# Optimization experiments

Measured on AMD Instinct MI355X. Metric: run time of the kernel, lower is better.

Reference implementation:

```python
import jax, jax.numpy as jnp
import numpy as np

B, C, W, H = 16, 512, 32, 32


def spatial_shift1(y):
    # y: [B, W, H, C]; quartile-wise shifts with edge rows/cols left unchanged
    c = y.shape[-1]
    cq = c // 4
    p0 = jnp.concatenate([y[:, :1, :, 0*cq:1*cq], y[:, :-1, :, 0*cq:1*cq]], axis=1)  # w <- w-1
    p1 = jnp.concatenate([y[:, 1:, :, 1*cq:2*cq], y[:, -1:, :, 1*cq:2*cq]], axis=1)  # w <- w+1
    p2 = jnp.concatenate([y[:, :, :1, 2*cq:3*cq], y[:, :, :-1, 2*cq:3*cq]], axis=2)  # h <- h-1
    p3 = jnp.concatenate([y[:, :, 1:, 3*cq:], y[:, :, -1:, 3*cq:]], axis=2)          # h <- h+1
    return jnp.concatenate([p0, p1, p2, p3], axis=-1)


def spatial_shift2(y):
    # same as shift1 with w/h roles swapped
    c = y.shape[-1]
    cq = c // 4
    p0 = jnp.concatenate([y[:, :, :1, 0*cq:1*cq], y[:, :, :-1, 0*cq:1*cq]], axis=2)  # h <- h-1
    p1 = jnp.concatenate([y[:, :, 1:, 1*cq:2*cq], y[:, :, -1:, 1*cq:2*cq]], axis=2)  # h <- h+1
    p2 = jnp.concatenate([y[:, :1, :, 2*cq:3*cq], y[:, :-1, :, 2*cq:3*cq]], axis=1)  # w <- w-1
    p3 = jnp.concatenate([y[:, 1:, :, 3*cq:], y[:, -1:, :, 3*cq:]], axis=1)          # w <- w+1
    return jnp.concatenate([p0, p1, p2, p3], axis=-1)


def setup_inputs() -> dict:
    key = jax.random.key(0)
    ks = jax.random.split(key, 9)
    s = 0.02
    return {
        "x": jax.random.normal(ks[0], (B, C, W, H), dtype=jnp.float32),
        "w1": jax.random.normal(ks[1], (3 * C, C), dtype=jnp.float32) * s,
        "b1": jax.random.normal(ks[2], (3 * C,), dtype=jnp.float32) * s,
        "wa": jax.random.normal(ks[3], (C, C), dtype=jnp.float32) * s,
        "ba": jax.random.normal(ks[4], (C,), dtype=jnp.float32) * s,
        "wb": jax.random.normal(ks[5], (3 * C, C), dtype=jnp.float32) * s,
        "bb": jax.random.normal(ks[6], (3 * C,), dtype=jnp.float32) * s,
        "w2": jax.random.normal(ks[7], (C, C), dtype=jnp.float32) * s,
        "b2": jax.random.normal(ks[8], (C,), dtype=jnp.float32) * s,
    }


def reference(x, w1, b1, wa, ba, wb, bb, w2, b2):
    c = x.shape[1]
    xp = jnp.transpose(x, (0, 2, 3, 1))                     # [B, W, H, C]
    y = jnp.einsum("bwhc,oc->bwho", xp, w1) + b1            # [B, W, H, 3C]
    x1 = spatial_shift1(y[..., :c])
    x2 = spatial_shift2(y[..., c:2 * c])
    x3 = y[..., 2 * c:]
    # SplitAttention: descriptor a = sum over branches and spatial positions
    a = jnp.sum(x1 + x2 + x3, axis=(1, 2))                  # [B, C]
    hat = jax.nn.gelu(a @ wa.T + ba, approximate=False) @ wb.T + bb  # [B, 3C]
    bar = jax.nn.softmax(hat.reshape(-1, 3, c), axis=1)     # softmax over k=3
    g = bar[:, :, None, None, :]                            # [B, 3, 1, 1, C]
    out = g[:, 0] * x1 + g[:, 1] * x2 + g[:, 2] * x3        # [B, W, H, C]
    z = jnp.einsum("bwhc,oc->bwho", out, w2) + b2           # [B, W, H, C]
    return jnp.transpose(z, (0, 3, 1, 2))                   # [B, C, W, H]
```

## Files before the change

### kernel.cpp

```cpp
#include <hip/hip_runtime.h>
#include <stdint.h>

typedef __bf16 bf16x8 __attribute__((ext_vector_type(8)));
typedef float f32x4 __attribute__((ext_vector_type(4)));

#define B_ 16
#define C_ 512
#define S_ 1024
#define N1 1536

__device__ inline unsigned short f2b(float f) {
    unsigned int u = __builtin_bit_cast(unsigned int, f);
    unsigned int lsb = (u >> 16) & 1u;
    u += 0x7fffu + lsb;
    return (unsigned short)(u >> 16);
}
__device__ inline float b2f(unsigned int s) {
    unsigned int u = (s & 0xffffu) << 16;
    return __builtin_bit_cast(float, u);
}

__device__ inline void gl_lds16(const unsigned short* g, unsigned short* l) {
    __builtin_amdgcn_global_load_lds(
        (const __attribute__((address_space(1))) void*)(g),
        (__attribute__((address_space(3))) void*)(l),
        16, 0, 0);
}

__global__ void transpose_convert_x(const float* __restrict__ x, unsigned short* __restrict__ xT) {
    __shared__ float tile[32][33];
    int b = blockIdx.z;
    int c0 = blockIdx.y * 32;
    int s0 = blockIdx.x * 32;
    int tx = threadIdx.x, ty = threadIdx.y;
    const float* xp = x + ((size_t)b * C_ + c0) * S_ + s0;
#pragma unroll
    for (int i = 0; i < 4; i++)
        tile[ty + i * 8][tx] = xp[(size_t)(ty + i * 8) * S_ + tx];
    __syncthreads();
    unsigned short* op = xT + ((size_t)b * S_ + s0) * C_ + c0;
#pragma unroll
    for (int i = 0; i < 4; i++)
        op[(size_t)(ty + i * 8) * C_ + tx] = f2b(tile[tx][ty + i * 8]);
}

__global__ __launch_bounds__(256) void misc_prep(
    const float* __restrict__ w1, const float* __restrict__ w2,
    unsigned short* __restrict__ w1b, unsigned short* __restrict__ w2b,
    float* __restrict__ sums)
{
    int i = blockIdx.x * 256 + threadIdx.x;
    if (i < 196608) {
        float4 v = ((const float4*)w1)[i];
        ((ushort4*)w1b)[i] = make_ushort4(f2b(v.x), f2b(v.y), f2b(v.z), f2b(v.w));
    } else if (i < 262144) {
        int j = i - 196608;
        float4 v = ((const float4*)w2)[j];
        ((ushort4*)w2b)[j] = make_ushort4(f2b(v.x), f2b(v.y), f2b(v.z), f2b(v.w));
    } else if (i < 292864) {
        int j = i - 262144;
        ((float4*)sums)[j] = make_float4(0.f, 0.f, 0.f, 0.f);
    }
}

template <bool TRANS_OUT, bool DO_SUMS>
__global__ __launch_bounds__(256) void gemm_bf16(
    const unsigned short* __restrict__ A,
    const unsigned short* __restrict__ Wt,
    const float* __restrict__ bias,
    void* __restrict__ Cout, int N,
    float* __restrict__ Tsum, float* __restrict__ H0, float* __restrict__ H31,
    float* __restrict__ C0, float* __restrict__ C31)
{
    const int K = 512;
    __shared__ __align__(16) unsigned short As[128 * 32];
    __shared__ __align__(16) unsigned short Bs[128 * 32];
    int m0 = blockIdx.x * 128;
    int n0 = blockIdx.y * 128;
    int tid = threadIdx.x;
    int lane = tid & 63, wid = tid >> 6;
    int wm = (wid >> 1) * 64, wn = (wid & 1) * 64;
    int quad = lane >> 4, l16 = lane & 15;
    int ch0 = wid * 128 + lane;
    const unsigned short* Ab = A + (size_t)m0 * K;
    const unsigned short* Bb = Wt + (size_t)n0 * K;

    f32x4 acc[4][4] = {};

    for (int kt = 0; kt < K; kt += 32) {
        __syncthreads();
#pragma unroll
        for (int i = 0; i < 2; i++) {
            int ch = ch0 + i * 64;
            int m = ch >> 2, kc = ch & 3;
            size_t go = (size_t)m * K + kt + kc * 8;
            gl_lds16(Ab + go, &As[ch * 8]);
            gl_lds16(Bb + go, &Bs[ch * 8]);
        }
        __syncthreads();
        bf16x8 af[4], bfr[4];
#pragma unroll
        for (int t = 0; t < 4; t++) {
            af[t]  = *(const bf16x8*)&As[(wm + t * 16 + l16) * 32 + quad * 8];
            bfr[t] = *(const bf16x8*)&Bs[(wn + t * 16 + l16) * 32 + quad * 8];
        }
#pragma unroll
        for (int mt = 0; mt < 4; mt++)
#pragma unroll
            for (int nt = 0; nt < 4; nt++)
                acc[mt][nt] = __builtin_amdgcn_mfma_f32_16x16x32_bf16(af[mt], bfr[nt], acc[mt][nt], 0, 0, 0);
    }

#pragma unroll
    for (int mt = 0; mt < 4; mt++) {
#pragma unroll
        for (int nt = 0; nt < 4; nt++) {
            int n = n0 + wn + nt * 16 + l16;
            float bv = bias[n];
            int mbase = m0 + wm + mt * 16 + quad * 4;
            if (!TRANS_OUT) {
                unsigned short* Y = (unsigned short*)Cout;
#pragma unroll
                for (int r = 0; r < 4; r++)
                    Y[(size_t)(mbase + r) * N + n] = f2b(acc[mt][nt][r] + bv);
            } else {
                float* Z = (float*)Cout;
                int b = mbase >> 10;
                int s = mbase & 1023;
                float4 v = make_float4(acc[mt][nt][0] + bv, acc[mt][nt][1] + bv,
                                       acc[mt][nt][2] + bv, acc[mt][nt][3] + bv);
                *(float4*)(&Z[((size_t)(b * 512 + n)) * 1024 + s]) = v;
            }
        }
    }

    if (DO_SUMS) {
        int b = m0 >> 10;
        int wlo = (m0 & 1023) >> 5;
#pragma unroll
        for (int nt = 0; nt < 4; nt++) {
            int n = n0 + wn + nt * 16 + l16;
            float bv = bias[n];
            float tT = 0.f;
#pragma unroll
            for (int mt = 0; mt < 4; mt++)
#pragma unroll
                for (int r = 0; r < 4; r++) tT += acc[mt][nt][r] + bv;
            tT += __shfl_xor(tT, 16);
            tT += __shfl_xor(tT, 32);
            if (quad == 0) {
                atomicAdd(&Tsum[b * 1536 + n], tT);
                float th0 = acc[0][nt][0] + acc[2][nt][0] + 2.f * bv;
                atomicAdd(&H0[b * 1536 + n], th0);
            }
            if (quad == 3) {
                float th31 = acc[1][nt][3] + acc[3][nt][3] + 2.f * bv;
                atomicAdd(&H31[b * 1536 + n], th31);
            }
            if (wlo == 0 && wm == 0) {
                float tc = 0.f;
#pragma unroll
                for (int mt = 0; mt < 2; mt++)
#pragma unroll
                    for (int r = 0; r < 4; r++) tc += acc[mt][nt][r] + bv;
                tc += __shfl_xor(tc, 16);
                tc += __shfl_xor(tc, 32);
                if (quad == 0) atomicAdd(&C0[b * 1536 + n], tc);
            }
            if (wlo == 28 && wm == 64) {
                float tc = 0.f;
#pragma unroll
                for (int mt = 2; mt < 4; mt++)
#pragma unroll
                    for (int r = 0; r < 4; r++) tc += acc[mt][nt][r] + bv;
                tc += __shfl_xor(tc, 16);
                tc += __shfl_xor(tc, 32);
                if (quad == 0) atomicAdd(&C31[b * 1536 + n], tc);
            }
        }
    }
}

__global__ __launch_bounds__(256) void mlp_layer1(
    const float* __restrict__ sums, const float* __restrict__ wa,
    const float* __restrict__ ba, float* __restrict__ h)
{
    __shared__ float sa[512];
    int b = blockIdx.x >> 7;
    int t = threadIdx.x;
    const float* Tp   = sums;
    const float* H0p  = sums + 24576;
    const float* H31p = sums + 49152;
    const float* C0p  = sums + 73728;
    const float* C31p = sums + 98304;
#pragma unroll
    for (int j = 0; j < 2; j++) {
        int c = t + j * 256;
        int q = c >> 7;
        int n1 = b * 1536 + c;
        float t123 = Tp[n1] + Tp[n1 + 512] + Tp[n1 + 1024];
        float sC1 = C0p[n1] - C31p[n1];
        float sH1 = H0p[n1] - H31p[n1];
        float sC2 = C0p[n1 + 512] - C31p[n1 + 512];
        float sH2 = H0p[n1 + 512] - H31p[n1 + 512];
        float e = (q < 2) ? (sC1 + sH2) : (sH1 + sC2);
        sa[c] = t123 + ((q & 1) ? -e : e);
    }
    __syncthreads();
    int lane = t & 63, wid = t >> 6;
    int o = (blockIdx.x & 127) * 4 + wid;
    const float4* wr = (const float4*)(wa + (size_t)o * 512);
    float4 w0 = wr[lane * 2], w1v = wr[lane * 2 + 1];
    float4 a0 = ((const float4*)sa)[lane * 2], a1 = ((const float4*)sa)[lane * 2 + 1];
    float dot = w0.x * a0.x + w0.y * a0.y + w0.z * a0.z + w0.w * a0.w
              + w1v.x * a1.x + w1v.y * a1.y + w1v.z * a1.z + w1v.w * a1.w;
#pragma unroll
    for (int off = 32; off; off >>= 1) dot += __shfl_down(dot, off);
    if (lane == 0) {
        float v = dot + ba[o];
        h[b * 512 + o] = 0.5f * v * (1.0f + erff(v * 0.7071067811865475f));
    }
}

__global__ __launch_bounds__(256) void mlp_layer2(
    const float* __restrict__ h, const float* __restrict__ wb,
    const float* __restrict__ bb, float* __restrict__ hat)
{
    int gw = (blockIdx.x * 256 + threadIdx.x) >> 6;
    int lane = threadIdx.x & 63;
    int b = gw / 1536;
    int o = gw - b * 1536;
    const float4* wr = (const float4*)(wb + (size_t)o * 512);
    const float4* hr = (const float4*)(h + (size_t)b * 512);
    float4 w0 = wr[lane * 2], w1 = wr[lane * 2 + 1];
    float4 h0 = hr[lane * 2], h1 = hr[lane * 2 + 1];
    float dot = w0.x * h0.x + w0.y * h0.y + w0.z * h0.z + w0.w * h0.w
              + w1.x * h1.x + w1.y * h1.y + w1.z * h1.z + w1.w * h1.w;
#pragma unroll
    for (int off = 32; off; off >>= 1) dot += __shfl_down(dot, off);
    if (lane == 0)
        hat[(size_t)b * 1536 + o] = dot + bb[o];
}

__global__ __launch_bounds__(256) void combine_softmax(
    const unsigned short* __restrict__ y, const float* __restrict__ hat,
    unsigned short* __restrict__ outT)
{
    int b = blockIdx.y;
    int t = threadIdx.x;
    int w = blockIdx.x * 4 + (t >> 6);
    int c8 = (t & 63) * 8;
    int q = c8 >> 7;
    int dw1 = (q == 0) ? -1 : (q == 1) ? 1 : 0;
    int dh1 = (q == 2) ? -1 : (q == 3) ? 1 : 0;
    int dh2 = (q == 0) ? -1 : (q == 1) ? 1 : 0;
    int dw2 = (q == 2) ? -1 : (q == 3) ? 1 : 0;
    float g0[8], g1[8], g2[8];
#pragma unroll
    for (int j = 0; j < 8; j++) {
        int c = c8 + j;
        float h0 = hat[b * 1536 + c];
        float h1 = hat[b * 1536 + 512 + c];
        float h2 = hat[b * 1536 + 1024 + c];
        float mx = fmaxf(h0, fmaxf(h1, h2));
        float e0 = __expf(h0 - mx), e1 = __expf(h1 - mx), e2 = __expf(h2 - mx);
        float inv = 1.0f / (e0 + e1 + e2);
        g0[j] = e0 * inv; g1[j] = e1 * inv; g2[j] = e2 * inv;
    }
    int w1i = min(max(w + dw1, 0), 31);
    int w2i = min(max(w + dw2, 0), 31);
    size_t base = (size_t)b * S_;
    for (int h = 0; h < 32; h++) {
        int h1i = min(max(h + dh1, 0), 31);
        int h2i = min(max(h + dh2, 0), 31);
        uint4 u1 = *(const uint4*)&y[(base + w1i * 32 + h1i) * N1 + c8];
        uint4 u2 = *(const uint4*)&y[(base + w2i * 32 + h2i) * N1 + 512 + c8];
        uint4 u3 = *(const uint4*)&y[(base + w * 32 + h) * N1 + 1024 + c8];
        unsigned int p[4];
        const unsigned int* a1 = &u1.x;
        const unsigned int* a2 = &u2.x;
        const unsigned int* a3 = &u3.x;
#pragma unroll
        for (int k = 0; k < 4; k++) {
            int j = k * 2;
            float lo = g0[j] * b2f(a1[k]) + g1[j] * b2f(a2[k]) + g2[j] * b2f(a3[k]);
            float hi = g0[j + 1] * b2f(a1[k] >> 16) + g1[j + 1] * b2f(a2[k] >> 16) + g2[j + 1] * b2f(a3[k] >> 16);
            p[k] = (unsigned int)f2b(lo) | ((unsigned int)f2b(hi) << 16);
        }
        *(uint4*)&outT[(base + w * 32 + h) * 512 + c8] = make_uint4(p[0], p[1], p[2], p[3]);
    }
}

extern "C" void kernel_launch(void* const* d_in, const int* in_sizes, int n_in,
                              void* d_out, int out_size, void* d_ws, size_t ws_size,
                              hipStream_t stream) {
    const float* x  = (const float*)d_in[0];
    const float* w1 = (const float*)d_in[1];
    const float* b1 = (const float*)d_in[2];
    const float* wa = (const float*)d_in[3];
    const float* ba = (const float*)d_in[4];
    const float* wb = (const float*)d_in[5];
    const float* bb = (const float*)d_in[6];
    const float* w2 = (const float*)d_in[7];
    const float* b2 = (const float*)d_in[8];
    float* out = (float*)d_out;

    char* ws = (char*)d_ws;
    unsigned short* xT   = (unsigned short*)(ws);
    unsigned short* outT = (unsigned short*)(ws);
    unsigned short* w1b  = (unsigned short*)(ws + 16777216);
    unsigned short* w2b  = (unsigned short*)(ws + 18350080);
    unsigned short* y    = (unsigned short*)(ws + 18874368);
    float* sums          = (float*)(ws + 69206016);
    float* h_buf         = (float*)(ws + 69697536);
    float* hat_buf       = (float*)(ws + 69730304);

    float* Tsum = sums;
    float* H0   = sums + 24576;
    float* H31  = sums + 49152;
    float* C0   = sums + 73728;
    float* C31  = sums + 98304;

    transpose_convert_x<<<dim3(32, 16, 16), dim3(32, 8), 0, stream>>>(x, xT);
    misc_prep<<<dim3(1144), dim3(256), 0, stream>>>(w1, w2, w1b, w2b, sums);
    gemm_bf16<false, true><<<dim3(128, 12), dim3(256), 0, stream>>>(
        xT, w1b, b1, (void*)y, 1536, Tsum, H0, H31, C0, C31);
    mlp_layer1<<<dim3(2048), dim3(256), 0, stream>>>(sums, wa, ba, h_buf);
    mlp_layer2<<<dim3(6144), dim3(256), 0, stream>>>(h_buf, wb, bb, hat_buf);
    combine_softmax<<<dim3(8, 16), dim3(256), 0, stream>>>(y, hat_buf, outT);
    gemm_bf16<true, false><<<dim3(128, 4), dim3(256), 0, stream>>>(
        outT, w2b, b2, (void*)out, 512, nullptr, nullptr, nullptr, nullptr, nullptr);
}
```

Measured before the change: 194.5 us.

## Widen GEMM K-tile with XOR-swizzled LDS, fuse prep kernels, parallelize combine

The GEMM now stages a 64-wide K slice per iteration and applies an XOR swizzle to the LDS layout. This halves the number of barrier pairs and is meant to avoid LDS bank conflicts on fragment reads. The weight-conversion and zeroing work is folded into the transpose kernel as an extra grid slice, which removes one kernel launch. combine_softmax now launches 4x more blocks, each covering 8 h-rows per wave instead of 32, to raise occupancy, at the cost of recomputing the softmax gates more often.

```diff
diff --git a/kernel.cpp b/kernel.cpp
--- a/kernel.cpp
+++ b/kernel.cpp
@@ -27,7 +27,29 @@
         16, 0, 0);
 }
 
-__global__ void transpose_convert_x(const float* __restrict__ x, unsigned short* __restrict__ xT) {
+__global__ void transpose_convert_x(const float* __restrict__ x, unsigned short* __restrict__ xT,
+                                    const float* __restrict__ w1, const float* __restrict__ w2,
+                                    unsigned short* __restrict__ w1b, unsigned short* __restrict__ w2b,
+                                    float* __restrict__ sums) {
+    if (blockIdx.z == 16) {
+        int t = (blockIdx.y * 32 + blockIdx.x) * 256 + threadIdx.y * 32 + threadIdx.x;
+#pragma unroll
+        for (int it = 0; it < 3; it++) {
+            int i = t + it * 131072;
+            if (i < 196608) {
+                float4 v = ((const float4*)w1)[i];
+                ((ushort4*)w1b)[i] = make_ushort4(f2b(v.x), f2b(v.y), f2b(v.z), f2b(v.w));
+            } else if (i < 262144) {
+                int j = i - 196608;
+                float4 v = ((const float4*)w2)[j];
+                ((ushort4*)w2b)[j] = make_ushort4(f2b(v.x), f2b(v.y), f2b(v.z), f2b(v.w));
+            } else if (i < 292864) {
+                int j = i - 262144;
+                ((float4*)sums)[j] = make_float4(0.f, 0.f, 0.f, 0.f);
+            }
+        }
+        return;
+    }
     __shared__ float tile[32][33];
     int b = blockIdx.z;
     int c0 = blockIdx.y * 32;
@@ -42,25 +64,6 @@
 #pragma unroll
     for (int i = 0; i < 4; i++)
         op[(size_t)(ty + i * 8) * C_ + tx] = f2b(tile[tx][ty + i * 8]);
-}
-
-__global__ __launch_bounds__(256) void misc_prep(
-    const float* __restrict__ w1, const float* __restrict__ w2,
-    unsigned short* __restrict__ w1b, unsigned short* __restrict__ w2b,
-    float* __restrict__ sums)
-{
-    int i = blockIdx.x * 256 + threadIdx.x;
-    if (i < 196608) {
-        float4 v = ((const float4*)w1)[i];
-        ((ushort4*)w1b)[i] = make_ushort4(f2b(v.x), f2b(v.y), f2b(v.z), f2b(v.w));
-    } else if (i < 262144) {
-        int j = i - 196608;
-        float4 v = ((const float4*)w2)[j];
-        ((ushort4*)w2b)[j] = make_ushort4(f2b(v.x), f2b(v.y), f2b(v.z), f2b(v.w));
-    } else if (i < 292864) {
-        int j = i - 262144;
-        ((float4*)sums)[j] = make_float4(0.f, 0.f, 0.f, 0.f);
-    }
 }
 
 template <bool TRANS_OUT, bool DO_SUMS>
@@ -73,42 +76,48 @@
     float* __restrict__ C0, float* __restrict__ C31)
 {
     const int K = 512;
-    __shared__ __align__(16) unsigned short As[128 * 32];
-    __shared__ __align__(16) unsigned short Bs[128 * 32];
+    __shared__ __align__(16) unsigned short As[128 * 64];
+    __shared__ __align__(16) unsigned short Bs[128 * 64];
     int m0 = blockIdx.x * 128;
     int n0 = blockIdx.y * 128;
     int tid = threadIdx.x;
     int lane = tid & 63, wid = tid >> 6;
     int wm = (wid >> 1) * 64, wn = (wid & 1) * 64;
     int quad = lane >> 4, l16 = lane & 15;
-    int ch0 = wid * 128 + lane;
     const unsigned short* Ab = A + (size_t)m0 * K;
     const unsigned short* Bb = Wt + (size_t)n0 * K;
 
     f32x4 acc[4][4] = {};
 
-    for (int kt = 0; kt < K; kt += 32) {
+    for (int kt = 0; kt < K; kt += 64) {
         __syncthreads();
 #pragma unroll
-        for (int i = 0; i < 2; i++) {
-            int ch = ch0 + i * 64;
-            int m = ch >> 2, kc = ch & 3;
+        for (int i = 0; i < 4; i++) {
+            int ch = i * 256 + tid;
+            int m = ch >> 3;
+            int kc = (ch & 7) ^ (m & 7);
             size_t go = (size_t)m * K + kt + kc * 8;
             gl_lds16(Ab + go, &As[ch * 8]);
             gl_lds16(Bb + go, &Bs[ch * 8]);
         }
         __syncthreads();
-        bf16x8 af[4], bfr[4];
-#pragma unroll
-        for (int t = 0; t < 4; t++) {
-            af[t]  = *(const bf16x8*)&As[(wm + t * 16 + l16) * 32 + quad * 8];
-            bfr[t] = *(const bf16x8*)&Bs[(wn + t * 16 + l16) * 32 + quad * 8];
-        }
-#pragma unroll
-        for (int mt = 0; mt < 4; mt++)
-#pragma unroll
-            for (int nt = 0; nt < 4; nt++)
-                acc[mt][nt] = __builtin_amdgcn_mfma_f32_16x16x32_bf16(af[mt], bfr[nt], acc[mt][nt], 0, 0, 0);
+#pragma unroll
+        for (int kh = 0; kh < 2; kh++) {
+            bf16x8 af[4], bfr[4];
+#pragma unroll
+            for (int t = 0; t < 4; t++) {
+                int ra = wm + t * 16 + l16;
+                int rb = wn + t * 16 + l16;
+                int kq = kh * 4 + quad;
+                af[t]  = *(const bf16x8*)&As[ra * 64 + ((kq ^ (ra & 7)) * 8)];
+                bfr[t] = *(const bf16x8*)&Bs[rb * 64 + ((kq ^ (rb & 7)) * 8)];
+            }
+#pragma unroll
+            for (int mt = 0; mt < 4; mt++)
+#pragma unroll
+                for (int nt = 0; nt < 4; nt++)
+                    acc[mt][nt] = __builtin_amdgcn_mfma_f32_16x16x32_bf16(af[mt], bfr[nt], acc[mt][nt], 0, 0, 0);
+        }
     }
 
 #pragma unroll
@@ -247,8 +256,9 @@
     unsigned short* __restrict__ outT)
 {
     int b = blockIdx.y;
+    int w = blockIdx.x;
     int t = threadIdx.x;
-    int w = blockIdx.x * 4 + (t >> 6);
+    int h0 = (t >> 6) * 8;
     int c8 = (t & 63) * 8;
     int q = c8 >> 7;
     int dw1 = (q == 0) ? -1 : (q == 1) ? 1 : 0;
@@ -259,18 +269,20 @@
 #pragma unroll
     for (int j = 0; j < 8; j++) {
         int c = c8 + j;
-        float h0 = hat[b * 1536 + c];
-        float h1 = hat[b * 1536 + 512 + c];
-        float h2 = hat[b * 1536 + 1024 + c];
-        float mx = fmaxf(h0, fmaxf(h1, h2));
-        float e0 = __expf(h0 - mx), e1 = __expf(h1 - mx), e2 = __expf(h2 - mx);
+        float h0v = hat[b * 1536 + c];
+        float h1v = hat[b * 1536 + 512 + c];
+        float h2v = hat[b * 1536 + 1024 + c];
+        float mx = fmaxf(h0v, fmaxf(h1v, h2v));
+        float e0 = __expf(h0v - mx), e1 = __expf(h1v - mx), e2 = __expf(h2v - mx);
         float inv = 1.0f / (e0 + e1 + e2);
         g0[j] = e0 * inv; g1[j] = e1 * inv; g2[j] = e2 * inv;
     }
     int w1i = min(max(w + dw1, 0), 31);
     int w2i = min(max(w + dw2, 0), 31);
     size_t base = (size_t)b * S_;
-    for (int h = 0; h < 32; h++) {
+#pragma unroll
+    for (int hh = 0; hh < 8; hh++) {
+        int h = h0 + hh;
         int h1i = min(max(h + dh1, 0), 31);
         int h2i = min(max(h + dh2, 0), 31);
         uint4 u1 = *(const uint4*)&y[(base + w1i * 32 + h1i) * N1 + c8];
@@ -321,13 +333,13 @@
     float* C0   = sums + 73728;
     float* C31  = sums + 98304;
 
-    transpose_convert_x<<<dim3(32, 16, 16), dim3(32, 8), 0, stream>>>(x, xT);
-    misc_prep<<<dim3(1144), dim3(256), 0, stream>>>(w1, w2, w1b, w2b, sums);
+    transpose_convert_x<<<dim3(32, 16, 17), dim3(32, 8), 0, stream>>>(
+        x, xT, w1, w2, w1b, w2b, sums);
     gemm_bf16<false, true><<<dim3(128, 12), dim3(256), 0, stream>>>(
         xT, w1b, b1, (void*)y, 1536, Tsum, H0, H31, C0, C31);
     mlp_layer1<<<dim3(2048), dim3(256), 0, stream>>>(sums, wa, ba, h_buf);
     mlp_layer2<<<dim3(6144), dim3(256), 0, stream>>>(h_buf, wb, bb, hat_buf);
-    combine_softmax<<<dim3(8, 16), dim3(256), 0, stream>>>(y, hat_buf, outT);
+    combine_softmax<<<dim3(32, 16), dim3(256), 0, stream>>>(y, hat_buf, outT);
     gemm_bf16<true, false><<<dim3(128, 4), dim3(256), 0, stream>>>(
         outT, w2b, b2, (void*)out, 512, nullptr, nullptr, nullptr, nullptr, nullptr);
 }
```

Result: faster. 180.3 us (-7.3%).
